# Kernel tuning notes

Measured on AMD Instinct MI355X. Metric: run time of the kernel, lower is better.

Reference implementation:

```python
import jax, jax.numpy as jnp
import numpy as np

B = 256      # graphs per batch
N = 512      # nodes per graph
FEAT = 64    # num_features
H = 64       # nhid
DEG = 16     # avg degree
RATIO = 0.5  # pooling_ratio
E = B * N * DEG


def setup_inputs() -> dict:
    key = jax.random.key(0)
    ks = jax.random.split(key, 12)
    # edges constructed within each graph via offsets
    src_loc = jax.random.randint(ks[0], (B, N * DEG), 0, N)
    dst_loc = jax.random.randint(ks[1], (B, N * DEG), 0, N)
    offs = (jnp.arange(B) * N)[:, None]
    edge_src = (src_loc + offs).reshape(-1).astype(jnp.int32)
    edge_dst = (dst_loc + offs).reshape(-1).astype(jnp.int32)
    batch = jnp.repeat(jnp.arange(B, dtype=jnp.int32), N)
    x = jax.random.normal(ks[2], (B * N, FEAT), dtype=jnp.float32)
    edge_attr = jax.random.uniform(ks[3], (E,), dtype=jnp.float32) + 0.1
    s1 = 1.0 / np.sqrt(FEAT)
    s2 = 1.0 / np.sqrt(H)
    return {
        "x": x,
        "edge_attr": edge_attr,
        "W1": jax.random.normal(ks[4], (FEAT, H), jnp.float32) * s1,
        "b1": jnp.zeros((H,), jnp.float32),
        "Wp1": jax.random.normal(ks[5], (H, 1), jnp.float32) * s2,
        "bp1": jnp.zeros((1,), jnp.float32),
        "W2": jax.random.normal(ks[6], (H, H), jnp.float32) * s2,
        "b2": jnp.zeros((H,), jnp.float32),
        "Wp2": jax.random.normal(ks[7], (H, 1), jnp.float32) * s2,
        "bp2": jnp.zeros((1,), jnp.float32),
        "edge_src": edge_src,
        "edge_dst": edge_dst,
        "batch": batch,
    }


def gcn_conv(x, W, b, src, dst, ew, n):
    """PyG GCNConv: sym-normalized weighted adjacency + self-loops (weight 1)."""
    h = x @ W                                   # [n, out]
    deg = jnp.zeros((n,), x.dtype).at[dst].add(ew) + 1.0  # self-loop adds 1
    dinv = jax.lax.rsqrt(deg)
    coef = dinv[dst] * ew * dinv[src]           # [E]
    out = jnp.zeros_like(h).at[dst].add(coef[:, None] * h[src])
    out = out + h * (1.0 / deg)[:, None]        # self-loop term: deg^-0.5 * 1 * deg^-0.5
    return out + b


def sag_pool(x, src, dst, ew, Wp, bp, n_per):
    """SAGPool: score = GCNConv(x)->1, per-graph top-k, gate by tanh(score),
    filter edges (dropped edges represented by zero weight)."""
    n = x.shape[0]
    score = gcn_conv(x, Wp, bp, src, dst, ew, n)[:, 0]   # [n]
    k = int(np.ceil(RATIO * n_per))
    _, idx = jax.lax.top_k(score.reshape(B, n_per), k)   # [B, k] local indices
    perm = (idx + (jnp.arange(B) * n_per)[:, None]).reshape(-1)
    xn = x[perm] * jnp.tanh(score[perm])[:, None]        # [B*k, H]
    newid = jnp.full((n,), -1, jnp.int32).at[perm].set(
        jnp.arange(B * k, dtype=jnp.int32))
    ns, nd = newid[src], newid[dst]
    valid = (ns >= 0) & (nd >= 0)
    ew2 = jnp.where(valid, ew, 0.0)
    ns = jnp.where(valid, ns, 0)
    nd = jnp.where(valid, nd, 0)
    return xn, ns, nd, ew2, k


def readout(x, k):
    """[gmp || gap] per graph; each graph has exactly k nodes, contiguous."""
    xg = x.reshape(B, k, -1)
    return jnp.concatenate([xg.max(axis=1), xg.mean(axis=1)], axis=1)  # [B, 2H]


def reference(x, edge_attr, W1, b1, Wp1, bp1, W2, b2, Wp2, bp2,
              edge_src, edge_dst, batch):
    n0 = x.shape[0]
    h = jax.nn.relu(gcn_conv(x, W1, b1, edge_src, edge_dst, edge_attr, n0))
    h, s1, d1, w1e, k1 = sag_pool(h, edge_src, edge_dst, edge_attr, Wp1, bp1, N)
    x1 = readout(h, k1)
    h = jax.nn.relu(gcn_conv(h, W2, b2, s1, d1, w1e, B * k1))
    h, _, _, _, k2 = sag_pool(h, s1, d1, w1e, Wp2, bp2, k1)
    x2 = readout(h, k2)
    return (x1 + x2) / 2.0
```

## Files before the change

### kernel.cpp

```cpp
#include <hip/hip_runtime.h>
#include <math.h>

#define BG   256
#define NN   512
#define EPG  (NN * 16)
#define NE   (BG * EPG)
#define N0   (BG * NN)
#define K1   256
#define N1_  (BG * K1)
#define K2   128
#define N2_  (BG * K2)

__device__ __forceinline__ float4 f4fma(float s, float4 a, float4 c) {
    c.x = fmaf(s, a.x, c.x); c.y = fmaf(s, a.y, c.y);
    c.z = fmaf(s, a.z, c.z); c.w = fmaf(s, a.w, c.w);
    return c;
}

template <int NPG, int K, bool REMAP, bool FINAL>
__global__ __launch_bounds__(1024)
void stage_kernel(const int* __restrict__ esrc, const int* __restrict__ edst,
                  const float* __restrict__ eatt, const int* __restrict__ nid_in,
                  int* __restrict__ nid_out,
                  int2* __restrict__ pairs, int* __restrict__ rowstart,
                  int* __restrict__ rowcnt, float* __restrict__ dinv,
                  const float4* __restrict__ X4, const float4* __restrict__ W4,
                  const float4* __restrict__ b4, const float4* __restrict__ wp4,
                  const float* __restrict__ bp,
                  float4* __restrict__ xn4, float* __restrict__ xr,
                  const float* __restrict__ x1r, float* __restrict__ out) {
    constexpr int PASSES = NPG / 32;
    constexpr int LPN = 1024 / NPG;
    constexpr int LOG_LPN = (LPN == 2) ? 1 : 2;
    constexpr int QF = 16 / LPN;
    constexpr int RLOG = (NPG == 512) ? 9 : 8;
    constexpr int RCH = NPG * NPG / 1024;
    constexpr int SH_A  = NPG * 68;
    constexpr int SH_UN = 4096;
    __shared__ __align__(16) float smem[SH_A + SH_UN + 2 * NPG + 64 + 64];
    float*  shx  = smem;
    int*    perm = (int*)(smem + SH_A);
    float*  shp  = smem + SH_A + NPG;
    float4* smx  = (float4*)(smem + SH_A);
    float4* ssm  = (float4*)(smem + SH_A + 2048);
    float*  ssc  = smem + SH_A + SH_UN;
    int*    rnk  = (int*)(smem + SH_A + SH_UN + NPG);
    float*  sbw  = smem + SH_A + SH_UN + 2 * NPG;
    int*    hist = (int*)(smem + SH_A + SH_UN + 2 * NPG + 64);
    int2*   lpair = (int2*)smem;
    int*    cnt   = (int*)smem + 8192;
    float*  wsum  = smem + 8192 + NPG;
    int*    scn   = (int*)smem + 8192 + 2 * NPG;
    float*  sdinv = smem + 8192 + 3 * NPG;
    int*    wtot  = (int*)smem + 8192 + 4 * NPG;
    float*  sWf   = smem + SH_A;

    int g = blockIdx.x, nbase = g * NPG, e0 = g * EPG;
    int t = threadIdx.x;
    int lane16 = t & 15, lane = t & 63;

    for (int i = t; i < NPG; i += 1024) { cnt[i] = 0; wsum[i] = 0.f; }
    __syncthreads();
    {
        const int4*   edst4 = (const int4*)(edst + e0);
        const int4*   esrc4 = (const int4*)(esrc + e0);
        const float4* eatt4 = (const float4*)(eatt + e0);
        int ed[8]; int es[8]; float ea[8];
#pragma unroll
        for (int c = 0; c < 2; ++c) {
            int ch = t + c * 1024;
            int4   dd = edst4[ch];
            int4   ss = esrc4[ch];
            float4 ww = eatt4[ch];
            ed[c * 4 + 0] = dd.x; ed[c * 4 + 1] = dd.y; ed[c * 4 + 2] = dd.z; ed[c * 4 + 3] = dd.w;
            es[c * 4 + 0] = ss.x; es[c * 4 + 1] = ss.y; es[c * 4 + 2] = ss.z; es[c * 4 + 3] = ss.w;
            ea[c * 4 + 0] = ww.x; ea[c * 4 + 1] = ww.y; ea[c * 4 + 2] = ww.z; ea[c * 4 + 3] = ww.w;
        }
        if (REMAP) {
#pragma unroll
            for (int j = 0; j < 8; ++j) { ed[j] = nid_in[ed[j]]; es[j] = nid_in[es[j]]; }
        }
#pragma unroll
        for (int j = 0; j < 8; ++j) {
            bool valid = !REMAP || (ed[j] >= 0 && es[j] >= 0);
            if (valid) {
                int dl = ed[j] - nbase;
                atomicAdd(&cnt[dl], 1);
                atomicAdd(&wsum[dl], ea[j]);
            }
        }
        __syncthreads();
        int wv = t >> 6;
        int xval = (t < NPG) ? cnt[t] : 0;
        int xs = xval;
#pragma unroll
        for (int off = 1; off < 64; off <<= 1) {
            int v = __shfl_up(xs, off, 64);
            if (lane >= off) xs += v;
        }
        if (lane == 63) wtot[wv] = xs;
        __syncthreads();
        int woff = 0, total = 0;
#pragma unroll
        for (int w = 0; w < 16; ++w) {
            int wt = wtot[w];
            if (w < wv) woff += wt;
            total += wt;
        }
        xs += woff;
        if (t < NPG) {
            int st = xs - xval;
            rowstart[nbase + t] = e0 + st;
            rowcnt[nbase + t]   = xval;
            float di = rsqrtf(wsum[t] + 1.0f);
            dinv[nbase + t] = di;
            sdinv[t] = di;
            scn[t] = st;
        }
        __syncthreads();
        int slots[8]; float cf[8];
#pragma unroll
        for (int j = 0; j < 8; ++j) {
            bool valid = !REMAP || (ed[j] >= 0 && es[j] >= 0);
            slots[j] = -1;
            if (valid) {
                int dl = ed[j] - nbase, sl = es[j] - nbase;
                cf[j] = sdinv[dl] * ea[j] * sdinv[sl];
                slots[j] = atomicAdd(&scn[dl], 1);
            }
        }
#pragma unroll
        for (int j = 0; j < 8; ++j)
            if (slots[j] >= 0 && slots[j] < 4096)
                lpair[slots[j]] = make_int2(es[j] - nbase, __float_as_int(cf[j]));
        __syncthreads();
        int n0 = total < 4096 ? total : 4096;
        for (int k2 = t; k2 < n0; k2 += 1024) pairs[e0 + k2] = lpair[k2];
        __syncthreads();
        if (total > 4096) {
#pragma unroll
            for (int j = 0; j < 8; ++j)
                if (slots[j] >= 4096)
                    lpair[slots[j] - 4096] = make_int2(es[j] - nbase, __float_as_int(cf[j]));
            __syncthreads();
            int n1 = total - 4096;
            for (int k2 = t; k2 < n1; k2 += 1024) pairs[e0 + 4096 + k2] = lpair[k2];
            __syncthreads();
        }
    }
    __syncthreads();

    for (int i = t; i < NPG * 16; i += 1024) {
        int r = i >> 4, c4 = i & 15;
        *(float4*)&shx[r * 68 + c4 * 4] = X4[(size_t)nbase * 16 + i];
    }
    {
        int r = t >> 4, c4 = t & 15;
        *(float4*)&sWf[r * 68 + c4 * 4] = W4[t];
    }
    __syncthreads();

    {
        constexpr int TILES = NPG / 64, TPG = TILES / 4;
        int q = t >> 8, tq = t & 255;
        int rg = tq >> 4, cg = tq & 15;
        float4 ac[TPG][4];
#pragma unroll
        for (int tt = 0; tt < TPG; ++tt) {
            int row0 = (tt * 4 + q) * 64;
            float4 acc0 = make_float4(0.f, 0.f, 0.f, 0.f);
            float4 acc1 = acc0, acc2 = acc0, acc3 = acc0;
#pragma unroll
            for (int k4 = 0; k4 < 16; ++k4) {
                float4 xv0 = *(const float4*)&shx[(row0 + rg * 4 + 0) * 68 + k4 * 4];
                float4 xv1 = *(const float4*)&shx[(row0 + rg * 4 + 1) * 68 + k4 * 4];
                float4 xv2 = *(const float4*)&shx[(row0 + rg * 4 + 2) * 68 + k4 * 4];
                float4 xv3 = *(const float4*)&shx[(row0 + rg * 4 + 3) * 68 + k4 * 4];
                float4 wv0 = *(const float4*)&sWf[(k4 * 4 + 0) * 68 + cg * 4];
                float4 wv1 = *(const float4*)&sWf[(k4 * 4 + 1) * 68 + cg * 4];
                float4 wv2 = *(const float4*)&sWf[(k4 * 4 + 2) * 68 + cg * 4];
                float4 wv3 = *(const float4*)&sWf[(k4 * 4 + 3) * 68 + cg * 4];
                acc0 = f4fma(xv0.x, wv0, acc0); acc0 = f4fma(xv0.y, wv1, acc0);
                acc0 = f4fma(xv0.z, wv2, acc0); acc0 = f4fma(xv0.w, wv3, acc0);
                acc1 = f4fma(xv1.x, wv0, acc1); acc1 = f4fma(xv1.y, wv1, acc1);
                acc1 = f4fma(xv1.z, wv2, acc1); acc1 = f4fma(xv1.w, wv3, acc1);
                acc2 = f4fma(xv2.x, wv0, acc2); acc2 = f4fma(xv2.y, wv1, acc2);
                acc2 = f4fma(xv2.z, wv2, acc2); acc2 = f4fma(xv2.w, wv3, acc2);
                acc3 = f4fma(xv3.x, wv0, acc3); acc3 = f4fma(xv3.y, wv1, acc3);
                acc3 = f4fma(xv3.z, wv2, acc3); acc3 = f4fma(xv3.w, wv3, acc3);
            }
            ac[tt][0] = acc0; ac[tt][1] = acc1; ac[tt][2] = acc2; ac[tt][3] = acc3;
        }
        __syncthreads();
#pragma unroll
        for (int tt = 0; tt < TPG; ++tt) {
            int row0 = (tt * 4 + q) * 64;
            *(float4*)&shx[(row0 + rg * 4 + 0) * 68 + cg * 4] = ac[tt][0];
            *(float4*)&shx[(row0 + rg * 4 + 1) * 68 + cg * 4] = ac[tt][1];
            *(float4*)&shx[(row0 + rg * 4 + 2) * 68 + cg * 4] = ac[tt][2];
            *(float4*)&shx[(row0 + rg * 4 + 3) * 68 + cg * 4] = ac[tt][3];
        }
    }
    if (t < 64) { sbw[t] = ((const float*)b4)[t]; hist[t] = 0; }
    for (int i = t; i < NPG; i += 1024) rnk[i] = 0;
    __syncthreads();

    for (int i = t; i < NPG; i += 1024) {
        int c = min(rowcnt[nbase + i], 63);
        atomicAdd(&hist[c], 1);
    }
    __syncthreads();
    if (t < 64) {
        int v = hist[t], s = v;
#pragma unroll
        for (int off = 1; off < 64; off <<= 1) {
            int u = __shfl_up(s, off, 64);
            if (lane >= off) s += u;
        }
        hist[t] = s - v;
    }
    __syncthreads();
    for (int i = t; i < NPG; i += 1024) {
        int c = min(rowcnt[nbase + i], 63);
        int pos = atomicAdd(&hist[c], 1);
        perm[pos] = i;
    }
    __syncthreads();
    {
        int idx2 = t >> LOG_LPN;
        int half = t & (LPN - 1);
        int nl = perm[idx2];
        int st = rowstart[nbase + nl], cn = rowcnt[nbase + nl];
        float di = dinv[nbase + nl], dii = di * di;
        int fb = half * QF;
        float4 acc[QF];
#pragma unroll
        for (int c = 0; c < QF; ++c) {
            float4 xv = *(const float4*)&shx[nl * 68 + (fb + c) * 4];
            acc[c].x = fmaf(xv.x, dii, sbw[(fb + c) * 4 + 0]);
            acc[c].y = fmaf(xv.y, dii, sbw[(fb + c) * 4 + 1]);
            acc[c].z = fmaf(xv.z, dii, sbw[(fb + c) * 4 + 2]);
            acc[c].w = fmaf(xv.w, dii, sbw[(fb + c) * 4 + 3]);
        }
        int2 p0 = (cn > 0) ? pairs[st] : make_int2(0, 0);
        int2 p1 = (cn > 1) ? pairs[st + 1] : make_int2(0, 0);
        for (int j = 0; j < cn; ++j) {
            int2 p2 = (j + 2 < cn) ? pairs[st + j + 2] : make_int2(0, 0);
            float cfv = __int_as_float(p0.y);
            int   s   = p0.x;
#pragma unroll
            for (int c = 0; c < QF; ++c)
                acc[c] = f4fma(cfv, *(const float4*)&shx[s * 68 + (fb + c) * 4], acc[c]);
            p0 = p1; p1 = p2;
        }
#pragma unroll
        for (int c = 0; c < QF; ++c) {
            acc[c].x = fmaxf(acc[c].x, 0.f); acc[c].y = fmaxf(acc[c].y, 0.f);
            acc[c].z = fmaxf(acc[c].z, 0.f); acc[c].w = fmaxf(acc[c].w, 0.f);
        }
        __syncthreads();
#pragma unroll
        for (int c = 0; c < QF; ++c)
            *(float4*)&shx[nl * 68 + (fb + c) * 4] = acc[c];
    }
    __syncthreads();
    if (t < 512) {
        int wv8 = t >> 6, sub4 = (t >> 4) & 3;
        float4 w4 = wp4[lane16];
#pragma unroll
        for (int p = 0; p < PASSES; ++p) {
            int n2 = p * 32 + wv8 * 4 + sub4;
            float4 a = *(const float4*)&shx[n2 * 68 + lane16 * 4];
            float tt = a.x * w4.x + a.y * w4.y + a.z * w4.z + a.w * w4.w;
            tt += __shfl_xor(tt, 1, 64); tt += __shfl_xor(tt, 2, 64);
            tt += __shfl_xor(tt, 4, 64); tt += __shfl_xor(tt, 8, 64);
            if (lane16 == 0) shp[n2] = tt;
        }
    }
    __syncthreads();
    if (t < NPG) {
        int i = perm[t];
        int st = rowstart[nbase + i], cn = rowcnt[nbase + i];
        float di = dinv[nbase + i];
        float a = fmaf(shp[i], di * di, bp[0]);
        int2 q0 = (cn > 0) ? pairs[st] : make_int2(0, 0);
        int2 q1 = (cn > 1) ? pairs[st + 1] : make_int2(0, 0);
        for (int j = 0; j < cn; ++j) {
            int2 q2 = (j + 2 < cn) ? pairs[st + j + 2] : make_int2(0, 0);
            a = fmaf(__int_as_float(q0.y), shp[q0.x], a);
            q0 = q1; q1 = q2;
        }
        ssc[i] = a;
    }
    __syncthreads();
    {
        int part = t >> RLOG;
        int i = t & (NPG - 1);
        float si = ssc[i];
        int j0 = part * RCH;
        int rank = 0;
        for (int j = j0; j < j0 + RCH; j += 4) {
            float4 sj = *(const float4*)&ssc[j];
            rank += (sj.x > si) || (sj.x == si && j     < i);
            rank += (sj.y > si) || (sj.y == si && j + 1 < i);
            rank += (sj.z > si) || (sj.z == si && j + 2 < i);
            rank += (sj.w > si) || (sj.w == si && j + 3 < i);
        }
        atomicAdd(&rnk[i], rank);
    }
    __syncthreads();
    if (!FINAL)
        for (int i = t; i < NPG; i += 1024)
            nid_out[nbase + i] = (rnk[i] < K) ? (g * K + rnk[i]) : -1;
    float4 mx = make_float4(-3.402823466e38f, -3.402823466e38f, -3.402823466e38f, -3.402823466e38f);
    float4 sm = make_float4(0.f, 0.f, 0.f, 0.f);
    if (t < 512) {
        int wv8 = t >> 6, sub4 = (t >> 4) & 3;
#pragma unroll
        for (int p = 0; p < PASSES; ++p) {
            int n2 = p * 32 + wv8 * 4 + sub4;
            int r = rnk[n2];
            if (r < K) {
                float gt = tanhf(ssc[n2]);
                float4 v = *(const float4*)&shx[n2 * 68 + lane16 * 4];
                v.x *= gt; v.y *= gt; v.z *= gt; v.w *= gt;
                if (!FINAL) xn4[((size_t)g * K + r) * 16 + lane16] = v;
                mx.x = fmaxf(mx.x, v.x); mx.y = fmaxf(mx.y, v.y);
                mx.z = fmaxf(mx.z, v.z); mx.w = fmaxf(mx.w, v.w);
                sm.x += v.x; sm.y += v.y; sm.z += v.z; sm.w += v.w;
            }
        }
    }
    int grp = t >> 4;
    __syncthreads();
    if (t < 512) {
        smx[grp * 16 + lane16] = mx;
        ssm[grp * 16 + lane16] = sm;
    }
    __syncthreads();
    if (grp == 0) {
#pragma unroll
        for (int u = 1; u < 32; ++u) {
            float4 a = smx[u * 16 + lane16], b = ssm[u * 16 + lane16];
            mx.x = fmaxf(mx.x, a.x); mx.y = fmaxf(mx.y, a.y);
            mx.z = fmaxf(mx.z, a.z); mx.w = fmaxf(mx.w, a.w);
            sm.x += b.x; sm.y += b.y; sm.z += b.z; sm.w += b.w;
        }
        float invK = 1.f / K;
        int c = lane16 * 4;
        float mr[4] = {mx.x, mx.y, mx.z, mx.w};
        float ar[4] = {sm.x * invK, sm.y * invK, sm.z * invK, sm.w * invK};
#pragma unroll
        for (int u = 0; u < 4; ++u) {
            if (FINAL) {
                out[g * 128 + c + u]      = 0.5f * (x1r[g * 128 + c + u]      + mr[u]);
                out[g * 128 + 64 + c + u] = 0.5f * (x1r[g * 128 + 64 + c + u] + ar[u]);
            } else {
                xr[g * 128 + c + u]      = mr[u];
                xr[g * 128 + 64 + c + u] = ar[u];
            }
        }
    }
}

extern "C" void kernel_launch(void* const* d_in, const int* in_sizes, int n_in,
                              void* d_out, int out_size, void* d_ws, size_t ws_size,
                              hipStream_t stream) {
    const float* x    = (const float*)d_in[0];
    const float* eatt = (const float*)d_in[1];
    const float* W1   = (const float*)d_in[2];
    const float* b1   = (const float*)d_in[3];
    const float* Wp1  = (const float*)d_in[4];
    const float* bp1  = (const float*)d_in[5];
    const float* W2   = (const float*)d_in[6];
    const float* b2   = (const float*)d_in[7];
    const float* Wp2  = (const float*)d_in[8];
    const float* bp2  = (const float*)d_in[9];
    const int*   esrc = (const int*)d_in[10];
    const int*   edst = (const int*)d_in[11];
    float* out = (float*)d_out;

    float* ws = (float*)d_ws;
    size_t o = 0;
    float* A    = ws + o; o += (size_t)N0 * 64;
    float* xn1  = ws + o; o += (size_t)N1_ * 64;
    int2*  prs  = (int2*)(ws + o); o += (size_t)NE * 2;
    int*   rst  = (int*)(ws + o); o += N0;
    int*   rcn  = (int*)(ws + o); o += N0;
    float* dinv = ws + o; o += N0;
    int*   nid  = (int*)(ws + o); o += N0;
    float* x1r  = ws + o; o += BG * 128;
    (void)A;

    stage_kernel<NN, K1, false, false><<<BG, 1024, 0, stream>>>(
        esrc, edst, eatt, nullptr, nid, prs, rst, rcn, dinv,
        (const float4*)x, (const float4*)W1, (const float4*)b1,
        (const float4*)Wp1, bp1, (float4*)xn1, x1r, nullptr, nullptr);
    stage_kernel<K1, K2, true, true><<<BG, 1024, 0, stream>>>(
        esrc, edst, eatt, nid, nullptr, prs, rst, rcn, dinv,
        (const float4*)xn1, (const float4*)W2, (const float4*)b2,
        (const float4*)Wp2, bp2, nullptr, nullptr, x1r, out);
}
```

Before: 207.2 us.

## Warp-specialize stage kernel to overlap CSR build with feature GEMM

Splits the 1024-thread block into two halves: threads 0-511 build the per-graph CSR (degree counts, scan, pair scatter) while threads 512-1023 load node features and compute the X·W GEMM in two phases, reading W from global instead of shared. Row start, count and dinv now live in shared memory instead of global arrays, and pairs are written directly to global rather than staged through shared. This aims to hide edge-processing latency behind the GEMM and remove global round-trips. In exchange, each half does twice the work per thread, register pressure rises, and the direct global pair scatter is uncoalesced.

```diff
diff --git a/kernel.cpp b/kernel.cpp
--- a/kernel.cpp
+++ b/kernel.cpp
@@ -9,7 +9,6 @@
 #define K1   256
 #define N1_  (BG * K1)
 #define K2   128
-#define N2_  (BG * K2)
 
 __device__ __forceinline__ float4 f4fma(float s, float4 a, float4 c) {
     c.x = fmaf(s, a.x, c.x); c.y = fmaf(s, a.y, c.y);
@@ -17,13 +16,38 @@
     return c;
 }
 
+__device__ __forceinline__ void gemm_tile(const float* __restrict__ shx,
+                                          const float4* __restrict__ W4,
+                                          int row0, int rg, int cg, float4 a[4]) {
+    float4 acc0 = make_float4(0.f, 0.f, 0.f, 0.f);
+    float4 acc1 = acc0, acc2 = acc0, acc3 = acc0;
+#pragma unroll
+    for (int k4 = 0; k4 < 16; ++k4) {
+        float4 xv0 = *(const float4*)&shx[(row0 + rg * 4 + 0) * 68 + k4 * 4];
+        float4 xv1 = *(const float4*)&shx[(row0 + rg * 4 + 1) * 68 + k4 * 4];
+        float4 xv2 = *(const float4*)&shx[(row0 + rg * 4 + 2) * 68 + k4 * 4];
+        float4 xv3 = *(const float4*)&shx[(row0 + rg * 4 + 3) * 68 + k4 * 4];
+        float4 wv0 = W4[(k4 * 4 + 0) * 16 + cg];
+        float4 wv1 = W4[(k4 * 4 + 1) * 16 + cg];
+        float4 wv2 = W4[(k4 * 4 + 2) * 16 + cg];
+        float4 wv3 = W4[(k4 * 4 + 3) * 16 + cg];
+        acc0 = f4fma(xv0.x, wv0, acc0); acc0 = f4fma(xv0.y, wv1, acc0);
+        acc0 = f4fma(xv0.z, wv2, acc0); acc0 = f4fma(xv0.w, wv3, acc0);
+        acc1 = f4fma(xv1.x, wv0, acc1); acc1 = f4fma(xv1.y, wv1, acc1);
+        acc1 = f4fma(xv1.z, wv2, acc1); acc1 = f4fma(xv1.w, wv3, acc1);
+        acc2 = f4fma(xv2.x, wv0, acc2); acc2 = f4fma(xv2.y, wv1, acc2);
+        acc2 = f4fma(xv2.z, wv2, acc2); acc2 = f4fma(xv2.w, wv3, acc2);
+        acc3 = f4fma(xv3.x, wv0, acc3); acc3 = f4fma(xv3.y, wv1, acc3);
+        acc3 = f4fma(xv3.z, wv2, acc3); acc3 = f4fma(xv3.w, wv3, acc3);
+    }
+    a[0] = acc0; a[1] = acc1; a[2] = acc2; a[3] = acc3;
+}
+
 template <int NPG, int K, bool REMAP, bool FINAL>
 __global__ __launch_bounds__(1024)
 void stage_kernel(const int* __restrict__ esrc, const int* __restrict__ edst,
                   const float* __restrict__ eatt, const int* __restrict__ nid_in,
-                  int* __restrict__ nid_out,
-                  int2* __restrict__ pairs, int* __restrict__ rowstart,
-                  int* __restrict__ rowcnt, float* __restrict__ dinv,
+                  int* __restrict__ nid_out, int2* __restrict__ pairs,
                   const float4* __restrict__ X4, const float4* __restrict__ W4,
                   const float4* __restrict__ b4, const float4* __restrict__ wp4,
                   const float* __restrict__ bp,
@@ -35,40 +59,44 @@
     constexpr int QF = 16 / LPN;
     constexpr int RLOG = (NPG == 512) ? 9 : 8;
     constexpr int RCH = NPG * NPG / 1024;
-    constexpr int SH_A  = NPG * 68;
-    constexpr int SH_UN = 4096;
-    __shared__ __align__(16) float smem[SH_A + SH_UN + 2 * NPG + 64 + 64];
-    float*  shx  = smem;
-    int*    perm = (int*)(smem + SH_A);
-    float*  shp  = smem + SH_A + NPG;
-    float4* smx  = (float4*)(smem + SH_A);
-    float4* ssm  = (float4*)(smem + SH_A + 2048);
-    float*  ssc  = smem + SH_A + SH_UN;
-    int*    rnk  = (int*)(smem + SH_A + SH_UN + NPG);
-    float*  sbw  = smem + SH_A + SH_UN + 2 * NPG;
-    int*    hist = (int*)(smem + SH_A + SH_UN + 2 * NPG + 64);
-    int2*   lpair = (int2*)smem;
-    int*    cnt   = (int*)smem + 8192;
-    float*  wsum  = smem + 8192 + NPG;
-    int*    scn   = (int*)smem + 8192 + 2 * NPG;
-    float*  sdinv = smem + 8192 + 3 * NPG;
-    int*    wtot  = (int*)smem + 8192 + 4 * NPG;
-    float*  sWf   = smem + SH_A;
+    constexpr int SH_A = NPG * 68;
+    constexpr int TILES = NPG / 64, TPP = TILES / 2, TB = TPP / 2 ? TPP / 2 : 1;
+    __shared__ __align__(16) float smem[SH_A + 4096 + 2 * NPG];
+    float* shx = smem;
+    float* S   = smem + SH_A;
+    int*   cnt   = (int*)S;
+    int*   rstl  = (int*)S + NPG;
+    float* sdinv = S + 2 * NPG;
+    int*   perm  = (int*)S + 3 * NPG;
+    float* shp   = S + 4 * NPG;
+    int*   scn   = (int*)S + 4 * NPG;
+    float* wsum  = S + 5 * NPG;
+    float* sbw   = S + 6 * NPG;
+    int*   hist  = (int*)S + 6 * NPG + 64;
+    int*   wtot  = (int*)S + 6 * NPG + 128;
+    float4* smx  = (float4*)S;
+    float4* ssm  = (float4*)(S + 2048);
+    float* ssc   = S + 4096;
+    int*   rnk   = (int*)S + 4096 + NPG;
 
     int g = blockIdx.x, nbase = g * NPG, e0 = g * EPG;
     int t = threadIdx.x;
     int lane16 = t & 15, lane = t & 63;
 
-    for (int i = t; i < NPG; i += 1024) { cnt[i] = 0; wsum[i] = 0.f; }
-    __syncthreads();
-    {
+    int ed[16], es[16]; float ea[16];
+    int xs = 0, xval = 0;
+    float4 accA[TB][4], accB[TB][4];
+    int tl = t - 512, q2 = (t & 511) >> 8, tq = t & 255;
+    int rgg = tq >> 4, cgg = tq & 15;
+
+    if (t < 512) {
+        for (int i = t; i < NPG; i += 512) { cnt[i] = 0; wsum[i] = 0.f; }
         const int4*   edst4 = (const int4*)(edst + e0);
         const int4*   esrc4 = (const int4*)(esrc + e0);
         const float4* eatt4 = (const float4*)(eatt + e0);
-        int ed[8]; int es[8]; float ea[8];
-#pragma unroll
-        for (int c = 0; c < 2; ++c) {
-            int ch = t + c * 1024;
+#pragma unroll
+        for (int c = 0; c < 4; ++c) {
+            int ch = t + c * 512;
             int4   dd = edst4[ch];
             int4   ss = esrc4[ch];
             float4 ww = eatt4[ch];
@@ -78,10 +106,20 @@
         }
         if (REMAP) {
 #pragma unroll
-            for (int j = 0; j < 8; ++j) { ed[j] = nid_in[ed[j]]; es[j] = nid_in[es[j]]; }
-        }
-#pragma unroll
-        for (int j = 0; j < 8; ++j) {
+            for (int j = 0; j < 16; ++j) { ed[j] = nid_in[ed[j]]; es[j] = nid_in[es[j]]; }
+        }
+    } else {
+        for (int i = tl; i < NPG * 16; i += 512) {
+            int r = i >> 4, c4 = i & 15;
+            *(float4*)&shx[r * 68 + c4 * 4] = X4[(size_t)nbase * 16 + i];
+        }
+        if (tl < 64) { sbw[tl] = ((const float*)b4)[tl]; hist[tl] = 0; }
+        for (int i = tl; i < NPG; i += 512) rnk[i] = 0;
+    }
+    __syncthreads();
+    if (t < 512) {
+#pragma unroll
+        for (int j = 0; j < 16; ++j) {
             bool valid = !REMAP || (ed[j] >= 0 && es[j] >= 0);
             if (valid) {
                 int dl = ed[j] - nbase;
@@ -89,124 +127,76 @@
                 atomicAdd(&wsum[dl], ea[j]);
             }
         }
-        __syncthreads();
-        int wv = t >> 6;
-        int xval = (t < NPG) ? cnt[t] : 0;
-        int xs = xval;
+    } else {
+#pragma unroll
+        for (int b = 0; b < TB; ++b)
+            gemm_tile(shx, W4, (q2 * TPP + b) * 64, rgg, cgg, accA[b]);
+    }
+    __syncthreads();
+    if (t < 512) {
+        int wvid = t >> 6;
+        xval = (t < NPG) ? cnt[t] : 0;
+        xs = xval;
 #pragma unroll
         for (int off = 1; off < 64; off <<= 1) {
             int v = __shfl_up(xs, off, 64);
             if (lane >= off) xs += v;
         }
-        if (lane == 63) wtot[wv] = xs;
-        __syncthreads();
-        int woff = 0, total = 0;
-#pragma unroll
-        for (int w = 0; w < 16; ++w) {
-            int wt = wtot[w];
-            if (w < wv) woff += wt;
-            total += wt;
-        }
+        if (lane == 63) wtot[wvid] = xs;
+    } else {
+#pragma unroll
+        for (int b = 0; b < TB; ++b) {
+            int row0 = (q2 * TPP + b) * 64;
+            *(float4*)&shx[(row0 + rgg * 4 + 0) * 68 + cgg * 4] = accA[b][0];
+            *(float4*)&shx[(row0 + rgg * 4 + 1) * 68 + cgg * 4] = accA[b][1];
+            *(float4*)&shx[(row0 + rgg * 4 + 2) * 68 + cgg * 4] = accA[b][2];
+            *(float4*)&shx[(row0 + rgg * 4 + 3) * 68 + cgg * 4] = accA[b][3];
+        }
+    }
+    __syncthreads();
+    if (t < 512) {
+        int wvid = t >> 6;
+        int woff = 0;
+#pragma unroll
+        for (int w = 0; w < 8; ++w) { int wt = wtot[w]; if (w < wvid) woff += wt; }
         xs += woff;
         if (t < NPG) {
             int st = xs - xval;
-            rowstart[nbase + t] = e0 + st;
-            rowcnt[nbase + t]   = xval;
-            float di = rsqrtf(wsum[t] + 1.0f);
-            dinv[nbase + t] = di;
-            sdinv[t] = di;
+            rstl[t] = st;
+            sdinv[t] = rsqrtf(wsum[t] + 1.0f);
             scn[t] = st;
         }
-        __syncthreads();
-        int slots[8]; float cf[8];
-#pragma unroll
-        for (int j = 0; j < 8; ++j) {
+    } else {
+#pragma unroll
+        for (int b = 0; b < TB; ++b)
+            gemm_tile(shx, W4, (q2 * TPP + TB + b) * 64, rgg, cgg, accB[b]);
+    }
+    __syncthreads();
+    if (t < 512) {
+#pragma unroll
+        for (int j = 0; j < 16; ++j) {
             bool valid = !REMAP || (ed[j] >= 0 && es[j] >= 0);
-            slots[j] = -1;
             if (valid) {
                 int dl = ed[j] - nbase, sl = es[j] - nbase;
-                cf[j] = sdinv[dl] * ea[j] * sdinv[sl];
-                slots[j] = atomicAdd(&scn[dl], 1);
+                float cf = sdinv[dl] * ea[j] * sdinv[sl];
+                int slot = atomicAdd(&scn[dl], 1);
+                pairs[e0 + slot] = make_int2(sl, __float_as_int(cf));
             }
         }
-#pragma unroll
-        for (int j = 0; j < 8; ++j)
-            if (slots[j] >= 0 && slots[j] < 4096)
-                lpair[slots[j]] = make_int2(es[j] - nbase, __float_as_int(cf[j]));
-        __syncthreads();
-        int n0 = total < 4096 ? total : 4096;
-        for (int k2 = t; k2 < n0; k2 += 1024) pairs[e0 + k2] = lpair[k2];
-        __syncthreads();
-        if (total > 4096) {
-#pragma unroll
-            for (int j = 0; j < 8; ++j)
-                if (slots[j] >= 4096)
-                    lpair[slots[j] - 4096] = make_int2(es[j] - nbase, __float_as_int(cf[j]));
-            __syncthreads();
-            int n1 = total - 4096;
-            for (int k2 = t; k2 < n1; k2 += 1024) pairs[e0 + 4096 + k2] = lpair[k2];
-            __syncthreads();
-        }
-    }
-    __syncthreads();
-
-    for (int i = t; i < NPG * 16; i += 1024) {
-        int r = i >> 4, c4 = i & 15;
-        *(float4*)&shx[r * 68 + c4 * 4] = X4[(size_t)nbase * 16 + i];
-    }
-    {
-        int r = t >> 4, c4 = t & 15;
-        *(float4*)&sWf[r * 68 + c4 * 4] = W4[t];
-    }
-    __syncthreads();
-
-    {
-        constexpr int TILES = NPG / 64, TPG = TILES / 4;
-        int q = t >> 8, tq = t & 255;
-        int rg = tq >> 4, cg = tq & 15;
-        float4 ac[TPG][4];
-#pragma unroll
-        for (int tt = 0; tt < TPG; ++tt) {
-            int row0 = (tt * 4 + q) * 64;
-            float4 acc0 = make_float4(0.f, 0.f, 0.f, 0.f);
-            float4 acc1 = acc0, acc2 = acc0, acc3 = acc0;
-#pragma unroll
-            for (int k4 = 0; k4 < 16; ++k4) {
-                float4 xv0 = *(const float4*)&shx[(row0 + rg * 4 + 0) * 68 + k4 * 4];
-                float4 xv1 = *(const float4*)&shx[(row0 + rg * 4 + 1) * 68 + k4 * 4];
-                float4 xv2 = *(const float4*)&shx[(row0 + rg * 4 + 2) * 68 + k4 * 4];
-                float4 xv3 = *(const float4*)&shx[(row0 + rg * 4 + 3) * 68 + k4 * 4];
-                float4 wv0 = *(const float4*)&sWf[(k4 * 4 + 0) * 68 + cg * 4];
-                float4 wv1 = *(const float4*)&sWf[(k4 * 4 + 1) * 68 + cg * 4];
-                float4 wv2 = *(const float4*)&sWf[(k4 * 4 + 2) * 68 + cg * 4];
-                float4 wv3 = *(const float4*)&sWf[(k4 * 4 + 3) * 68 + cg * 4];
-                acc0 = f4fma(xv0.x, wv0, acc0); acc0 = f4fma(xv0.y, wv1, acc0);
-                acc0 = f4fma(xv0.z, wv2, acc0); acc0 = f4fma(xv0.w, wv3, acc0);
-                acc1 = f4fma(xv1.x, wv0, acc1); acc1 = f4fma(xv1.y, wv1, acc1);
-                acc1 = f4fma(xv1.z, wv2, acc1); acc1 = f4fma(xv1.w, wv3, acc1);
-                acc2 = f4fma(xv2.x, wv0, acc2); acc2 = f4fma(xv2.y, wv1, acc2);
-                acc2 = f4fma(xv2.z, wv2, acc2); acc2 = f4fma(xv2.w, wv3, acc2);
-                acc3 = f4fma(xv3.x, wv0, acc3); acc3 = f4fma(xv3.y, wv1, acc3);
-                acc3 = f4fma(xv3.z, wv2, acc3); acc3 = f4fma(xv3.w, wv3, acc3);
-            }
-            ac[tt][0] = acc0; ac[tt][1] = acc1; ac[tt][2] = acc2; ac[tt][3] = acc3;
-        }
-        __syncthreads();
-#pragma unroll
-        for (int tt = 0; tt < TPG; ++tt) {
-            int row0 = (tt * 4 + q) * 64;
-            *(float4*)&shx[(row0 + rg * 4 + 0) * 68 + cg * 4] = ac[tt][0];
-            *(float4*)&shx[(row0 + rg * 4 + 1) * 68 + cg * 4] = ac[tt][1];
-            *(float4*)&shx[(row0 + rg * 4 + 2) * 68 + cg * 4] = ac[tt][2];
-            *(float4*)&shx[(row0 + rg * 4 + 3) * 68 + cg * 4] = ac[tt][3];
-        }
-    }
-    if (t < 64) { sbw[t] = ((const float*)b4)[t]; hist[t] = 0; }
-    for (int i = t; i < NPG; i += 1024) rnk[i] = 0;
+    } else {
+#pragma unroll
+        for (int b = 0; b < TB; ++b) {
+            int row0 = (q2 * TPP + TB + b) * 64;
+            *(float4*)&shx[(row0 + rgg * 4 + 0) * 68 + cgg * 4] = accB[b][0];
+            *(float4*)&shx[(row0 + rgg * 4 + 1) * 68 + cgg * 4] = accB[b][1];
+            *(float4*)&shx[(row0 + rgg * 4 + 2) * 68 + cgg * 4] = accB[b][2];
+            *(float4*)&shx[(row0 + rgg * 4 + 3) * 68 + cgg * 4] = accB[b][3];
+        }
+    }
     __syncthreads();
 
     for (int i = t; i < NPG; i += 1024) {
-        int c = min(rowcnt[nbase + i], 63);
+        int c = min(cnt[i], 63);
         atomicAdd(&hist[c], 1);
     }
     __syncthreads();
@@ -221,7 +211,7 @@
     }
     __syncthreads();
     for (int i = t; i < NPG; i += 1024) {
-        int c = min(rowcnt[nbase + i], 63);
+        int c = min(cnt[i], 63);
         int pos = atomicAdd(&hist[c], 1);
         perm[pos] = i;
     }
@@ -230,8 +220,9 @@
         int idx2 = t >> LOG_LPN;
         int half = t & (LPN - 1);
         int nl = perm[idx2];
-        int st = rowstart[nbase + nl], cn = rowcnt[nbase + nl];
-        float di = dinv[nbase + nl], dii = di * di;
+        int st = rstl[nl], cn = cnt[nl];
+        float di = sdinv[nl], dii = di * di;
+        const int2* pb = pairs + e0 + st;
         int fb = half * QF;
         float4 acc[QF];
 #pragma unroll
@@ -242,10 +233,10 @@
             acc[c].z = fmaf(xv.z, dii, sbw[(fb + c) * 4 + 2]);
             acc[c].w = fmaf(xv.w, dii, sbw[(fb + c) * 4 + 3]);
         }
-        int2 p0 = (cn > 0) ? pairs[st] : make_int2(0, 0);
-        int2 p1 = (cn > 1) ? pairs[st + 1] : make_int2(0, 0);
+        int2 p0 = (cn > 0) ? pb[0] : make_int2(0, 0);
+        int2 p1 = (cn > 1) ? pb[1] : make_int2(0, 0);
         for (int j = 0; j < cn; ++j) {
-            int2 p2 = (j + 2 < cn) ? pairs[st + j + 2] : make_int2(0, 0);
+            int2 p2 = (j + 2 < cn) ? pb[j + 2] : make_int2(0, 0);
             float cfv = __int_as_float(p0.y);
             int   s   = p0.x;
 #pragma unroll
@@ -280,15 +271,16 @@
     __syncthreads();
     if (t < NPG) {
         int i = perm[t];
-        int st = rowstart[nbase + i], cn = rowcnt[nbase + i];
-        float di = dinv[nbase + i];
+        int st = rstl[i], cn = cnt[i];
+        float di = sdinv[i];
+        const int2* pb = pairs + e0 + st;
         float a = fmaf(shp[i], di * di, bp[0]);
-        int2 q0 = (cn > 0) ? pairs[st] : make_int2(0, 0);
-        int2 q1 = (cn > 1) ? pairs[st + 1] : make_int2(0, 0);
+        int2 q0 = (cn > 0) ? pb[0] : make_int2(0, 0);
+        int2 q1 = (cn > 1) ? pb[1] : make_int2(0, 0);
         for (int j = 0; j < cn; ++j) {
-            int2 q2 = (j + 2 < cn) ? pairs[st + j + 2] : make_int2(0, 0);
+            int2 q2v = (j + 2 < cn) ? pb[j + 2] : make_int2(0, 0);
             a = fmaf(__int_as_float(q0.y), shp[q0.x], a);
-            q0 = q1; q1 = q2;
+            q0 = q1; q1 = q2v;
         }
         ssc[i] = a;
     }
@@ -390,14 +382,14 @@
     float* dinv = ws + o; o += N0;
     int*   nid  = (int*)(ws + o); o += N0;
     float* x1r  = ws + o; o += BG * 128;
-    (void)A;
+    (void)A; (void)rst; (void)rcn; (void)dinv;
 
     stage_kernel<NN, K1, false, false><<<BG, 1024, 0, stream>>>(
-        esrc, edst, eatt, nullptr, nid, prs, rst, rcn, dinv,
+        esrc, edst, eatt, nullptr, nid, prs,
         (const float4*)x, (const float4*)W1, (const float4*)b1,
         (const float4*)Wp1, bp1, (float4*)xn1, x1r, nullptr, nullptr);
     stage_kernel<K1, K2, true, true><<<BG, 1024, 0, stream>>>(
-        esrc, edst, eatt, nid, nullptr, prs, rst, rcn, dinv,
+        esrc, edst, eatt, nid, nullptr, prs,
         (const float4*)xn1, (const float4*)W2, (const float4*)b2,
         (const float4*)Wp2, bp2, nullptr, nullptr, x1r, out);
 }
```

New measurement: 257.3 us. 24.2% more time.
